# Optimization experiments

Measured on AMD Instinct MI355X. Metric: run time of the kernel, lower is better.

## Reference

```python
import jax, jax.numpy as jnp
import numpy as np

B, C, H, W = 4, 256, 64, 64
C8 = C // 8


def setup_inputs() -> dict:
    key = jax.random.key(0)
    ks = jax.random.split(key, 8)
    x = jax.random.normal(ks[0], (B, C, H, W), dtype=jnp.float32)
    # 1x1 conv weights act as per-pixel linear maps: [out_ch, in_ch]
    Wq = jax.random.normal(ks[1], (C8, C), dtype=jnp.float32) * 0.05
    bq = jax.random.normal(ks[2], (C8,), dtype=jnp.float32) * 0.01
    Wk = jax.random.normal(ks[3], (C8, C), dtype=jnp.float32) * 0.05
    bk = jax.random.normal(ks[4], (C8,), dtype=jnp.float32) * 0.01
    Wv = jax.random.normal(ks[5], (C, C), dtype=jnp.float32) * 0.05
    bv = jax.random.normal(ks[6], (C,), dtype=jnp.float32) * 0.01
    # torch inits gamma to 0 (identity); use nonzero so output exercises the attention path
    gamma = jnp.array(0.5, dtype=jnp.float32)
    return {"x": x, "Wq": Wq, "bq": bq, "Wk": Wk, "bk": bk, "Wv": Wv, "bv": bv, "gamma": gamma}


def reference(x, Wq, bq, Wk, bk, Wv, bv, gamma):
    b, c, h, w = x.shape
    n = h * w
    xf = x.reshape(b, c, n)                                   # [B,C,N]
    q = jnp.einsum('oc,bcn->bno', Wq, xf) + bq                # [B,N,C8] (proj_query permuted)
    k = jnp.einsum('oc,bcn->bon', Wk, xf) + bk[:, None]       # [B,C8,N]
    energy = jnp.einsum('bnc,bcm->bnm', q, k)                 # [B,N_q,N_k]
    # NOTE: torch Softmax(dim=1) -> normalize over the QUERY axis (axis=1)
    attention = jax.nn.softmax(energy, axis=1)
    v = jnp.einsum('oc,bcn->bon', Wv, xf) + bv[:, None]       # [B,C,N]
    out = jnp.einsum('bcn,bnm->bcm', v, attention).reshape(b, c, h, w)
    return gamma * out + x
```

## Files before the change

kernel.cpp:

```cpp
#include <hip/hip_runtime.h>
#include <hip/hip_bf16.h>

#define BN 4
#define CC 256
#define C8 32
#define NN 4096
#define PROJ_ROWS 320

typedef __attribute__((ext_vector_type(8))) short short8;
typedef __attribute__((ext_vector_type(4))) float f32x4;

__device__ __forceinline__ unsigned short f2bf(float f) {
    unsigned u = __builtin_bit_cast(unsigned, f);
    unsigned r = (u + 0x7fffu + ((u >> 16) & 1u)) >> 16;
    return (unsigned short)r;
}

__global__ __launch_bounds__(256) void proj_kernel(
    const float* __restrict__ x,
    const float* __restrict__ Wq, const float* __restrict__ bq,
    const float* __restrict__ Wk, const float* __restrict__ bk,
    const float* __restrict__ Wv, const float* __restrict__ bv,
    unsigned short* __restrict__ proj, unsigned short* __restrict__ qT)
{
    int bid = blockIdx.x;
    int b = bid >> 6, nt = bid & 63;
    int n0 = nt * 64;
    int tid = threadIdx.x;
    int w = tid >> 6, l = tid & 63, l15 = l & 15, lq = l >> 4;

    __shared__ alignas(16) unsigned short Xt[64][264];

    int c_l = tid >> 3;
    int nb  = (tid & 7) * 8;

#pragma unroll
    for (int kc = 0; kc < 8; kc++) {
        const float* xp = x + ((size_t)(b * CC + kc * 32 + c_l)) * NN + n0 + nb;
        float4 x0 = *(const float4*)xp;
        float4 x1 = *(const float4*)(xp + 4);
        float t[8] = {x0.x, x0.y, x0.z, x0.w, x1.x, x1.y, x1.z, x1.w};
#pragma unroll
        for (int e = 0; e < 8; e++) Xt[nb + e][kc * 32 + c_l] = f2bf(t[e]);
    }
    __syncthreads();

    f32x4 acc[5][4];
#pragma unroll
    for (int gi = 0; gi < 5; gi++)
#pragma unroll
        for (int mi = 0; mi < 4; mi++) acc[gi][mi] = (f32x4){0.f, 0.f, 0.f, 0.f};

    for (int kc = 0; kc < 8; kc++) {
        float4 wf[5][2];
#pragma unroll
        for (int gi = 0; gi < 5; gi++) {
            int og = (w * 5 + gi) * 16 + l15;
            const float* wrow = (og < 32) ? (Wq + (size_t)og * CC)
                              : (og < 64) ? (Wk + (size_t)(og - 32) * CC)
                                          : (Wv + (size_t)(og - 64) * CC);
            const float* wp = wrow + kc * 32 + lq * 8;
            wf[gi][0] = *(const float4*)wp;
            wf[gi][1] = *(const float4*)(wp + 4);
        }
#pragma unroll
        for (int gi = 0; gi < 5; gi++) {
            unsigned short a8[8] __attribute__((aligned(16)));
            float tw[8] = {wf[gi][0].x, wf[gi][0].y, wf[gi][0].z, wf[gi][0].w,
                           wf[gi][1].x, wf[gi][1].y, wf[gi][1].z, wf[gi][1].w};
#pragma unroll
            for (int e = 0; e < 8; e++) a8[e] = f2bf(tw[e]);
            short8 af = *(const short8*)a8;
#pragma unroll
            for (int mi = 0; mi < 4; mi++) {
                short8 bf = *(const short8*)&Xt[mi * 16 + l15][kc * 32 + lq * 8];
                acc[gi][mi] = __builtin_amdgcn_mfma_f32_16x16x32_bf16(af, bf, acc[gi][mi], 0, 0, 0);
            }
        }
    }

#pragma unroll
    for (int gi = 0; gi < 5; gi++) {
#pragma unroll
        for (int r = 0; r < 4; r++) {
            int og = (w * 5 + gi) * 16 + lq * 4 + r;
            float bias = (og < 32) ? bq[og] : (og < 64) ? bk[og - 32] : bv[og - 64];
#pragma unroll
            for (int mi = 0; mi < 4; mi++) {
                int n = n0 + mi * 16 + l15;
                unsigned short v16 = f2bf(acc[gi][mi][r] + bias);
                if (og < 32) {
                    qT[((size_t)b * NN + n) * C8 + og] = v16;
                } else {
                    proj[((size_t)b * PROJ_ROWS + og) * NN + n] = v16;
                }
            }
        }
    }
}

template<int NSPLIT, bool FINAL>
__global__ __launch_bounds__(256, 4) void attn_kernel(
    const unsigned short* __restrict__ proj,
    const unsigned short* __restrict__ qT,
    const float* __restrict__ x,
    const float* __restrict__ gamma_p,
    float* __restrict__ out,
    float* __restrict__ Opart,
    float* __restrict__ Lpart)
{
    constexpr int ITERS = 64 / NSPLIT;
    int bid = blockIdx.x;
    int h   = bid >> 8;
    int low = bid & 255;
    int xcd = low & 7;
    int b = xcd >> 1;
    int mtile = ((low >> 3) << 1) | (xcd & 1);
    int m0 = mtile * 64;
    int nbase = h * (ITERS * 64);

    int tid = threadIdx.x;
    int w = tid >> 6, l = tid & 63, l15 = l & 15, lq = l >> 4;

    __shared__ alignas(16) unsigned short ps[2][64][72];
    __shared__ float red[4][64];
    __shared__ float Ltot[64];

    const unsigned short* kbase = proj + ((size_t)b * PROJ_ROWS + C8) * NN;
    const unsigned short* vbase = proj + ((size_t)b * PROJ_ROWS + 64) * NN;
    const unsigned short* qbase = qT + (size_t)b * NN * C8;

    short8 kfrag[4];
#pragma unroll
    for (int mi = 0; mi < 4; mi++) {
        int col = m0 + mi * 16 + l15;
        unsigned short t8[8] __attribute__((aligned(16)));
#pragma unroll
        for (int j = 0; j < 8; j++)
            t8[j] = kbase[(size_t)(lq * 8 + j) * NN + col];
        kfrag[mi] = *(const short8*)t8;
    }

    f32x4 O[4][4];
#pragma unroll
    for (int ci = 0; ci < 4; ci++)
#pragma unroll
        for (int mi = 0; mi < 4; mi++) O[ci][mi] = (f32x4){0.f, 0.f, 0.f, 0.f};
    float runS[4] = {0.f, 0.f, 0.f, 0.f};

    {
        short8 qfrag = *(const short8*)(qbase + (size_t)(nbase + 16 * w + l15) * C8 + lq * 8);
#pragma unroll
        for (int mi = 0; mi < 4; mi++) {
            f32x4 S = __builtin_amdgcn_mfma_f32_16x16x32_bf16(
                qfrag, kfrag[mi], (f32x4){0.f, 0.f, 0.f, 0.f}, 0, 0, 0);
            float p0 = __expf(S[0]);
            float p1 = __expf(S[1]);
            float p2 = __expf(S[2]);
            float p3 = __expf(S[3]);
            runS[mi] += (p0 + p1) + (p2 + p3);
            unsigned pk0 = (unsigned)f2bf(p0) | ((unsigned)f2bf(p1) << 16);
            unsigned pk1 = (unsigned)f2bf(p2) | ((unsigned)f2bf(p3) << 16);
            *(uint2*)&ps[0][mi * 16 + l15][16 * w + lq * 4] = make_uint2(pk0, pk1);
        }
    }

    for (int it = 0; it < ITERS; it++) {
        int n0c = nbase + it * 64;
        __syncthreads();

        const unsigned short* psrc = &ps[it & 1][0][0];
#pragma unroll
        for (int kh = 0; kh < 2; kh++) {
            short8 av[4];
#pragma unroll
            for (int ci = 0; ci < 4; ci++)
                av[ci] = *(const short8*)(vbase
                         + (size_t)(64 * w + ci * 16 + l15) * NN + n0c + kh * 32 + lq * 8);
            short8 bfr[4];
#pragma unroll
            for (int mi = 0; mi < 4; mi++)
                bfr[mi] = *(const short8*)(psrc + (mi * 16 + l15) * 72 + kh * 32 + lq * 8);
#pragma unroll
            for (int ci = 0; ci < 4; ci++)
#pragma unroll
                for (int mi = 0; mi < 4; mi++)
                    O[ci][mi] = __builtin_amdgcn_mfma_f32_16x16x32_bf16(
                        av[ci], bfr[mi], O[ci][mi], 0, 0, 0);
        }

        if (it + 1 < ITERS) {
            short8 qfrag = *(const short8*)(qbase
                           + (size_t)(n0c + 64 + 16 * w + l15) * C8 + lq * 8);
            unsigned short* pdst = &ps[(it + 1) & 1][0][0];
#pragma unroll
            for (int mi = 0; mi < 4; mi++) {
                f32x4 S = __builtin_amdgcn_mfma_f32_16x16x32_bf16(
                    qfrag, kfrag[mi], (f32x4){0.f, 0.f, 0.f, 0.f}, 0, 0, 0);
                float p0 = __expf(S[0]);
                float p1 = __expf(S[1]);
                float p2 = __expf(S[2]);
                float p3 = __expf(S[3]);
                runS[mi] += (p0 + p1) + (p2 + p3);
                unsigned pk0 = (unsigned)f2bf(p0) | ((unsigned)f2bf(p1) << 16);
                unsigned pk1 = (unsigned)f2bf(p2) | ((unsigned)f2bf(p3) << 16);
                *(uint2*)(pdst + (mi * 16 + l15) * 72 + 16 * w + lq * 4) = make_uint2(pk0, pk1);
            }
        }
    }

#pragma unroll
    for (int mi = 0; mi < 4; mi++) {
        float s = runS[mi];
        s += __shfl_xor(s, 16);
        s += __shfl_xor(s, 32);
        red[w][mi * 16 + l15] = s;
    }
    __syncthreads();
    if (tid < 64) Ltot[tid] = red[0][tid] + red[1][tid] + red[2][tid] + red[3][tid];
    __syncthreads();

    if constexpr (FINAL) {
        float gamma = gamma_p[0];
        float iv[4];
#pragma unroll
        for (int mi = 0; mi < 4; mi++) iv[mi] = 1.0f / Ltot[mi * 16 + l15];
#pragma unroll
        for (int ci = 0; ci < 4; ci++) {
#pragma unroll
            for (int mi = 0; mi < 4; mi++) {
                int m = m0 + mi * 16 + l15;
#pragma unroll
                for (int r = 0; r < 4; r++) {
                    int c = 64 * w + ci * 16 + lq * 4 + r;
                    size_t idx = ((size_t)b * CC + c) * NN + m;
                    out[idx] = gamma * (O[ci][mi][r] * iv[mi]) + x[idx];
                }
            }
        }
    } else {
        size_t p = ((size_t)h * BN + b) * 64 + mtile;
        if (tid < 64) Lpart[p * 64 + tid] = Ltot[tid];
        float* Ob = Opart + p * (size_t)(CC * 64);
#pragma unroll
        for (int ci = 0; ci < 4; ci++) {
#pragma unroll
            for (int mi = 0; mi < 4; mi++) {
#pragma unroll
                for (int r = 0; r < 4; r++) {
                    int c = 64 * w + ci * 16 + lq * 4 + r;
                    Ob[c * 64 + mi * 16 + l15] = O[ci][mi][r];
                }
            }
        }
    }
}

template<int NSPLIT>
__global__ __launch_bounds__(256) void combine_kernel(
    const float* __restrict__ Opart, const float* __restrict__ Lpart,
    const float* __restrict__ x, const float* __restrict__ gamma_p,
    float* __restrict__ out)
{
    int bid = blockIdx.x;
    int cq = bid & 3;
    int mt = (bid >> 2) & 63;
    int b  = bid >> 8;
    int tid = threadIdx.x;
    int m4 = tid & 15, c16 = tid >> 4;
    float gamma = gamma_p[0];

    f32x4 Ls = (f32x4){0.f, 0.f, 0.f, 0.f};
#pragma unroll
    for (int h = 0; h < NSPLIT; h++) {
        size_t p = ((size_t)h * BN + b) * 64 + mt;
        Ls += *(const f32x4*)(Lpart + p * 64 + m4 * 4);
    }
    f32x4 inv;
#pragma unroll
    for (int j = 0; j < 4; j++) inv[j] = 1.0f / Ls[j];

#pragma unroll
    for (int cp = 0; cp < 4; cp++) {
        int c = cq * 64 + cp * 16 + c16;
        f32x4 acc = (f32x4){0.f, 0.f, 0.f, 0.f};
#pragma unroll
        for (int h = 0; h < NSPLIT; h++) {
            size_t p = ((size_t)h * BN + b) * 64 + mt;
            acc += *(const f32x4*)(Opart + p * (size_t)(CC * 64) + c * 64 + m4 * 4);
        }
        size_t idx = ((size_t)b * CC + c) * NN + mt * 64 + m4 * 4;
        f32x4 xv = *(const f32x4*)(x + idx);
        f32x4 o;
#pragma unroll
        for (int j = 0; j < 4; j++) o[j] = gamma * (acc[j] * inv[j]) + xv[j];
        *(f32x4*)(out + idx) = o;
    }
}

extern "C" void kernel_launch(void* const* d_in, const int* in_sizes, int n_in,
                              void* d_out, int out_size, void* d_ws, size_t ws_size,
                              hipStream_t stream) {
    const float* x     = (const float*)d_in[0];
    const float* Wq    = (const float*)d_in[1];
    const float* bq    = (const float*)d_in[2];
    const float* Wk    = (const float*)d_in[3];
    const float* bk    = (const float*)d_in[4];
    const float* Wv    = (const float*)d_in[5];
    const float* bv    = (const float*)d_in[6];
    const float* gamma = (const float*)d_in[7];
    float* out = (float*)d_out;
    (void)in_sizes; (void)n_in; (void)out_size;

    unsigned short* proj = (unsigned short*)d_ws;
    unsigned short* qT   = proj + (size_t)BN * PROJ_ROWS * NN;
    const size_t baseB = ((size_t)BN * PROJ_ROWS * NN + (size_t)BN * NN * C8) * 2;

    auto needB = [&](int ns) {
        size_t LpB = (size_t)ns * BN * 64 * 64 * 4;
        size_t OpB = (size_t)ns * BN * 64 * CC * 64 * 4;
        return baseB + LpB + OpB;
    };

    proj_kernel<<<256, 256, 0, stream>>>(x, Wq, bq, Wk, bk, Wv, bv, proj, qT);

    if (ws_size >= needB(4)) {
        float* Lpart = (float*)((char*)d_ws + baseB);
        float* Opart = Lpart + (size_t)4 * BN * 64 * 64;
        attn_kernel<4, false><<<1024, 256, 0, stream>>>(proj, qT, x, gamma, out, Opart, Lpart);
        combine_kernel<4><<<1024, 256, 0, stream>>>(Opart, Lpart, x, gamma, out);
    } else if (ws_size >= needB(2)) {
        float* Lpart = (float*)((char*)d_ws + baseB);
        float* Opart = Lpart + (size_t)2 * BN * 64 * 64;
        attn_kernel<2, false><<<512, 256, 0, stream>>>(proj, qT, x, gamma, out, Opart, Lpart);
        combine_kernel<2><<<1024, 256, 0, stream>>>(Opart, Lpart, x, gamma, out);
    } else {
        attn_kernel<1, true><<<256, 256, 0, stream>>>(proj, qT, x, gamma, out, nullptr, nullptr);
    }
}
```

Baseline: 180.4 us.

## Process 128 keys per attention iteration, raise MFMA priority, vectorize partial stores

The attention loop now fills a 128-wide probability tile per barrier instead of 64, halving the number of __syncthreads and outer iterations and enlarging the LDS buffer. s_setprio is raised around the PV MFMA block so matrix work is favored over the exp/softmax phase of other waves. The partial O layout is changed to store whole f32x4 MFMA fragments contiguously, and the combine kernel is rewritten to read that layout and write scalar outputs. The larger shared tile uses more LDS per block, which may reduce occupancy.

Measured after the change: 191.2 us. +6.0%, slower.

```diff
diff --git a/kernel.cpp b/kernel.cpp
--- a/kernel.cpp
+++ b/kernel.cpp
@@ -109,7 +109,8 @@
     float* __restrict__ Opart,
     float* __restrict__ Lpart)
 {
-    constexpr int ITERS = 64 / NSPLIT;
+    constexpr int ITERS  = 64 / NSPLIT;
+    constexpr int OITERS = ITERS / 2;
     int bid = blockIdx.x;
     int h   = bid >> 8;
     int low = bid & 255;
@@ -122,7 +123,7 @@
     int tid = threadIdx.x;
     int w = tid >> 6, l = tid & 63, l15 = l & 15, lq = l >> 4;
 
-    __shared__ alignas(16) unsigned short ps[2][64][72];
+    __shared__ alignas(16) unsigned short ps[2][64][136];
     __shared__ float red[4][64];
     __shared__ float Ltot[64];
 
@@ -148,8 +149,10 @@
         for (int mi = 0; mi < 4; mi++) O[ci][mi] = (f32x4){0.f, 0.f, 0.f, 0.f};
     float runS[4] = {0.f, 0.f, 0.f, 0.f};
 
-    {
-        short8 qfrag = *(const short8*)(qbase + (size_t)(nbase + 16 * w + l15) * C8 + lq * 8);
+#pragma unroll
+    for (int t = 0; t < 2; t++) {
+        short8 qfrag = *(const short8*)(qbase
+                       + (size_t)(nbase + t * 64 + 16 * w + l15) * C8 + lq * 8);
 #pragma unroll
         for (int mi = 0; mi < 4; mi++) {
             f32x4 S = __builtin_amdgcn_mfma_f32_16x16x32_bf16(
@@ -161,17 +164,17 @@
             runS[mi] += (p0 + p1) + (p2 + p3);
             unsigned pk0 = (unsigned)f2bf(p0) | ((unsigned)f2bf(p1) << 16);
             unsigned pk1 = (unsigned)f2bf(p2) | ((unsigned)f2bf(p3) << 16);
-            *(uint2*)&ps[0][mi * 16 + l15][16 * w + lq * 4] = make_uint2(pk0, pk1);
-        }
-    }
-
-    for (int it = 0; it < ITERS; it++) {
-        int n0c = nbase + it * 64;
+            *(uint2*)&ps[0][mi * 16 + l15][t * 64 + 16 * w + lq * 4] = make_uint2(pk0, pk1);
+        }
+    }
+
+    for (int it = 0; it < OITERS; it++) {
+        int n0c = nbase + it * 128;
         __syncthreads();
 
         const unsigned short* psrc = &ps[it & 1][0][0];
 #pragma unroll
-        for (int kh = 0; kh < 2; kh++) {
+        for (int kh = 0; kh < 4; kh++) {
             short8 av[4];
 #pragma unroll
             for (int ci = 0; ci < 4; ci++)
@@ -180,31 +183,37 @@
             short8 bfr[4];
 #pragma unroll
             for (int mi = 0; mi < 4; mi++)
-                bfr[mi] = *(const short8*)(psrc + (mi * 16 + l15) * 72 + kh * 32 + lq * 8);
+                bfr[mi] = *(const short8*)(psrc + (mi * 16 + l15) * 136 + kh * 32 + lq * 8);
+            __builtin_amdgcn_s_setprio(1);
 #pragma unroll
             for (int ci = 0; ci < 4; ci++)
 #pragma unroll
                 for (int mi = 0; mi < 4; mi++)
                     O[ci][mi] = __builtin_amdgcn_mfma_f32_16x16x32_bf16(
                         av[ci], bfr[mi], O[ci][mi], 0, 0, 0);
-        }
-
-        if (it + 1 < ITERS) {
-            short8 qfrag = *(const short8*)(qbase
-                           + (size_t)(n0c + 64 + 16 * w + l15) * C8 + lq * 8);
+            __builtin_amdgcn_s_setprio(0);
+        }
+
+        if (it + 1 < OITERS) {
             unsigned short* pdst = &ps[(it + 1) & 1][0][0];
 #pragma unroll
-            for (int mi = 0; mi < 4; mi++) {
-                f32x4 S = __builtin_amdgcn_mfma_f32_16x16x32_bf16(
-                    qfrag, kfrag[mi], (f32x4){0.f, 0.f, 0.f, 0.f}, 0, 0, 0);
-                float p0 = __expf(S[0]);
-                float p1 = __expf(S[1]);
-                float p2 = __expf(S[2]);
-                float p3 = __expf(S[3]);
-                runS[mi] += (p0 + p1) + (p2 + p3);
-                unsigned pk0 = (unsigned)f2bf(p0) | ((unsigned)f2bf(p1) << 16);
-                unsigned pk1 = (unsigned)f2bf(p2) | ((unsigned)f2bf(p3) << 16);
-                *(uint2*)(pdst + (mi * 16 + l15) * 72 + 16 * w + lq * 4) = make_uint2(pk0, pk1);
+            for (int t = 0; t < 2; t++) {
+                short8 qfrag = *(const short8*)(qbase
+                               + (size_t)(n0c + 128 + t * 64 + 16 * w + l15) * C8 + lq * 8);
+#pragma unroll
+                for (int mi = 0; mi < 4; mi++) {
+                    f32x4 S = __builtin_amdgcn_mfma_f32_16x16x32_bf16(
+                        qfrag, kfrag[mi], (f32x4){0.f, 0.f, 0.f, 0.f}, 0, 0, 0);
+                    float p0 = __expf(S[0]);
+                    float p1 = __expf(S[1]);
+                    float p2 = __expf(S[2]);
+                    float p3 = __expf(S[3]);
+                    runS[mi] += (p0 + p1) + (p2 + p3);
+                    unsigned pk0 = (unsigned)f2bf(p0) | ((unsigned)f2bf(p1) << 16);
+                    unsigned pk1 = (unsigned)f2bf(p2) | ((unsigned)f2bf(p3) << 16);
+                    *(uint2*)(pdst + (mi * 16 + l15) * 136 + t * 64 + 16 * w + lq * 4)
+                        = make_uint2(pk0, pk1);
+                }
             }
         }
     }
@@ -246,11 +255,8 @@
         for (int ci = 0; ci < 4; ci++) {
 #pragma unroll
             for (int mi = 0; mi < 4; mi++) {
-#pragma unroll
-                for (int r = 0; r < 4; r++) {
-                    int c = 64 * w + ci * 16 + lq * 4 + r;
-                    Ob[c * 64 + mi * 16 + l15] = O[ci][mi][r];
-                }
+                int quad = 16 * w + ci * 4 + lq;
+                *(f32x4*)&Ob[((size_t)quad * 64 + mi * 16 + l15) * 4] = O[ci][mi];
             }
         }
     }
@@ -267,34 +273,33 @@
     int mt = (bid >> 2) & 63;
     int b  = bid >> 8;
     int tid = threadIdx.x;
-    int m4 = tid & 15, c16 = tid >> 4;
+    int m = tid & 63, qo = tid >> 6;
     float gamma = gamma_p[0];
 
-    f32x4 Ls = (f32x4){0.f, 0.f, 0.f, 0.f};
+    float Ls = 0.f;
 #pragma unroll
     for (int h = 0; h < NSPLIT; h++) {
         size_t p = ((size_t)h * BN + b) * 64 + mt;
-        Ls += *(const f32x4*)(Lpart + p * 64 + m4 * 4);
-    }
-    f32x4 inv;
-#pragma unroll
-    for (int j = 0; j < 4; j++) inv[j] = 1.0f / Ls[j];
+        Ls += Lpart[p * 64 + m];
+    }
+    float inv = 1.0f / Ls;
 
 #pragma unroll
     for (int cp = 0; cp < 4; cp++) {
-        int c = cq * 64 + cp * 16 + c16;
+        int quad = cq * 16 + cp * 4 + qo;
         f32x4 acc = (f32x4){0.f, 0.f, 0.f, 0.f};
 #pragma unroll
         for (int h = 0; h < NSPLIT; h++) {
             size_t p = ((size_t)h * BN + b) * 64 + mt;
-            acc += *(const f32x4*)(Opart + p * (size_t)(CC * 64) + c * 64 + m4 * 4);
-        }
-        size_t idx = ((size_t)b * CC + c) * NN + mt * 64 + m4 * 4;
-        f32x4 xv = *(const f32x4*)(x + idx);
-        f32x4 o;
-#pragma unroll
-        for (int j = 0; j < 4; j++) o[j] = gamma * (acc[j] * inv[j]) + xv[j];
-        *(f32x4*)(out + idx) = o;
+            acc += *(const f32x4*)(Opart + p * (size_t)(CC * 64)
+                                   + ((size_t)quad * 64 + m) * 4);
+        }
+#pragma unroll
+        for (int r = 0; r < 4; r++) {
+            int c = quad * 4 + r;
+            size_t idx = ((size_t)b * CC + c) * NN + mt * 64 + m;
+            out[idx] = gamma * (acc[r] * inv) + x[idx];
+        }
     }
 }
 
```
